# Kernel tuning notes

Measured on AMD Instinct MI355X. Metric: run time of the kernel, lower is better.

## Reference

```python
import jax, jax.numpy as jnp
import numpy as np

B, D, O = 131072, 128, 256

def setup_inputs() -> dict:
    key = jax.random.key(0)
    k1, k2, k3 = jax.random.split(key, 3)
    x = jax.random.normal(k1, (B, D), dtype=jnp.float32)
    weight = jax.random.normal(k2, (O, D), dtype=jnp.float32)
    bias = jax.random.normal(k3, (O,), dtype=jnp.float32)
    return {"x": x, "weight": weight, "bias": bias}

def reference(x, weight, bias):
    # Original: (x[:,None,:] * W[None,:,:]).sum(-1) == linear contraction over D.
    z = jnp.einsum('bd,od->bo', x, weight) + bias  # [B, O]
    # hyperoperation_order == 2 -> elementwise square; activation is None.
    return z * z
```

## Files before the change

kernel.cpp:

```cpp
#include <hip/hip_runtime.h>
#include <hip/hip_bf16.h>


#define B_ROWS 131072
#define D_DIM  128
#define O_DIM  256
#define ROWS_PER_BLOCK 128
#define THREADS 512
#define W_PITCH 136

using bf16x8 = __attribute__((ext_vector_type(8))) short;
using f32x4  = __attribute__((ext_vector_type(4))) float;

__device__ __forceinline__ short bf16bits(float f) {
    __hip_bfloat16 h = __float2bfloat16(f);
    return __builtin_bit_cast(short, h);
}

__global__ __launch_bounds__(THREADS, 4)
void hyper_linear_sq_kernel(const float* __restrict__ x,
                            const float* __restrict__ weight,
                            const float* __restrict__ bias,
                            float* __restrict__ out) {
    __shared__ short Wlds[O_DIM * W_PITCH];

    const int tid = threadIdx.x;

    {
        const float4* wv = (const float4*)weight;
        #pragma unroll
        for (int it = 0; it < 16; ++it) {
            int idx = it * THREADS + tid;
            float4 v = wv[idx];
            int e   = idx << 2;
            int row = e >> 7;
            int c   = e & 127;
            short4 p;
            p.x = bf16bits(v.x); p.y = bf16bits(v.y);
            p.z = bf16bits(v.z); p.w = bf16bits(v.w);
            *(short4*)&Wlds[row * W_PITCH + c] = p;
        }
    }

    const int lane = tid & 63;
    const int wid  = tid >> 6;
    const int n16  = lane & 15;
    const int quad = lane >> 4;

    const long rowbase = (long)blockIdx.x * ROWS_PER_BLOCK + wid * 16;

    const float* xr = x + (rowbase + n16) * D_DIM + quad * 8;
    bf16x8 a[4];
    #pragma unroll
    for (int ks = 0; ks < 4; ++ks) {
        float4 h0 = *(const float4*)(xr + ks * 32);
        float4 h1 = *(const float4*)(xr + ks * 32 + 4);
        bf16x8 t;
        t[0] = bf16bits(h0.x); t[1] = bf16bits(h0.y);
        t[2] = bf16bits(h0.z); t[3] = bf16bits(h0.w);
        t[4] = bf16bits(h1.x); t[5] = bf16bits(h1.y);
        t[6] = bf16bits(h1.z); t[7] = bf16bits(h1.w);
        a[ks] = t;
    }

    f32x4 acc[16];
    #pragma unroll
    for (int ct = 0; ct < 16; ++ct) acc[ct] = (f32x4){0.f, 0.f, 0.f, 0.f};

    __syncthreads();

    #pragma unroll
    for (int ks = 0; ks < 4; ++ks) {
        #pragma unroll
        for (int ct = 0; ct < 16; ++ct) {
            bf16x8 b = *(const bf16x8*)&Wlds[(ct * 16 + n16) * W_PITCH + ks * 32 + quad * 8];
            acc[ct] = __builtin_amdgcn_mfma_f32_16x16x32_bf16(a[ks], b, acc[ct], 0, 0, 0);
        }
    }

    #pragma unroll
    for (int ct = 0; ct < 16; ++ct) {
        int col = ct * 16 + n16;
        float bv = bias[col];
        #pragma unroll
        for (int r = 0; r < 4; ++r) {
            long row = rowbase + quad * 4 + r;
            float z = acc[ct][r] + bv;
            out[row * O_DIM + col] = z * z;
        }
    }
}

extern "C" void kernel_launch(void* const* d_in, const int* in_sizes, int n_in,
                              void* d_out, int out_size, void* d_ws, size_t ws_size,
                              hipStream_t stream) {
    const float* x    = (const float*)d_in[0];
    const float* w    = (const float*)d_in[1];
    const float* bias = (const float*)d_in[2];
    float* out        = (float*)d_out;
    dim3 grid(B_ROWS / ROWS_PER_BLOCK);
    hipLaunchKernelGGL(hyper_linear_sq_kernel, grid, dim3(THREADS), 0, stream,
                       x, w, bias, out);
}
```

Baseline: 189.1 us.

## Hold weight fragments in registers per wave, drop LDS, split columns across waves

Stops staging the full weight matrix in LDS. Each of four waves now owns 64 output columns and keeps its bf16 weight fragments and bias in registers, then loops over four 16-row tiles of x. This removes the LDS fill, the block barrier and the LDS reads. In exchange, every wave reloads the same x rows (four times per block) and reads weight from global or L2 once per block. It also replaces the library bf16 conversion with a manual round-to-nearest-even bit trick.

New measurement: 229.6 us. +21.4%, slower.

```diff
diff --git a/kernel.cpp b/kernel.cpp
--- a/kernel.cpp
+++ b/kernel.cpp
@@ -5,88 +5,91 @@
 #define B_ROWS 131072
 #define D_DIM  128
 #define O_DIM  256
-#define ROWS_PER_BLOCK 128
-#define THREADS 512
-#define W_PITCH 136
+#define THREADS 256
+#define NBLOCKS 2048
+#define ROWS_PER_BLOCK 64
+#define TILES (ROWS_PER_BLOCK / 16)
 
 using bf16x8 = __attribute__((ext_vector_type(8))) short;
 using f32x4  = __attribute__((ext_vector_type(4))) float;
 
-__device__ __forceinline__ short bf16bits(float f) {
-    __hip_bfloat16 h = __float2bfloat16(f);
-    return __builtin_bit_cast(short, h);
+__device__ __forceinline__ short bf16rne(float f) {
+    unsigned u = __builtin_bit_cast(unsigned, f);
+    u += 0x7FFFu + ((u >> 16) & 1u);
+    return (short)(u >> 16);
 }
 
-__global__ __launch_bounds__(THREADS, 4)
+__device__ __forceinline__ bf16x8 pack8(float4 h0, float4 h1) {
+    bf16x8 t;
+    t[0] = bf16rne(h0.x); t[1] = bf16rne(h0.y);
+    t[2] = bf16rne(h0.z); t[3] = bf16rne(h0.w);
+    t[4] = bf16rne(h1.x); t[5] = bf16rne(h1.y);
+    t[6] = bf16rne(h1.z); t[7] = bf16rne(h1.w);
+    return t;
+}
+
+__global__ __launch_bounds__(THREADS, 3)
 void hyper_linear_sq_kernel(const float* __restrict__ x,
                             const float* __restrict__ weight,
                             const float* __restrict__ bias,
                             float* __restrict__ out) {
-    __shared__ short Wlds[O_DIM * W_PITCH];
+    const int lane  = threadIdx.x & 63;
+    const int wid   = threadIdx.x >> 6;
+    const int n16   = lane & 15;
+    const int quad  = lane >> 4;
+    const int cbase = wid * 64;
 
-    const int tid = threadIdx.x;
-
-    {
-        const float4* wv = (const float4*)weight;
+    bf16x8 bfrag[4][4];
+    #pragma unroll
+    for (int ct = 0; ct < 4; ++ct) {
+        const float* wr = weight + (cbase + ct * 16 + n16) * D_DIM + quad * 8;
         #pragma unroll
-        for (int it = 0; it < 16; ++it) {
-            int idx = it * THREADS + tid;
-            float4 v = wv[idx];
-            int e   = idx << 2;
-            int row = e >> 7;
-            int c   = e & 127;
-            short4 p;
-            p.x = bf16bits(v.x); p.y = bf16bits(v.y);
-            p.z = bf16bits(v.z); p.w = bf16bits(v.w);
-            *(short4*)&Wlds[row * W_PITCH + c] = p;
+        for (int ks = 0; ks < 4; ++ks) {
+            float4 h0 = *(const float4*)(wr + ks * 32);
+            float4 h1 = *(const float4*)(wr + ks * 32 + 4);
+            bfrag[ct][ks] = pack8(h0, h1);
         }
     }
 
-    const int lane = tid & 63;
-    const int wid  = tid >> 6;
-    const int n16  = lane & 15;
-    const int quad = lane >> 4;
+    float bv[4];
+    #pragma unroll
+    for (int ct = 0; ct < 4; ++ct) bv[ct] = bias[cbase + ct * 16 + n16];
 
-    const long rowbase = (long)blockIdx.x * ROWS_PER_BLOCK + wid * 16;
+    const int rowbase0 = blockIdx.x * ROWS_PER_BLOCK;
 
-    const float* xr = x + (rowbase + n16) * D_DIM + quad * 8;
-    bf16x8 a[4];
-    #pragma unroll
-    for (int ks = 0; ks < 4; ++ks) {
-        float4 h0 = *(const float4*)(xr + ks * 32);
-        float4 h1 = *(const float4*)(xr + ks * 32 + 4);
-        bf16x8 t;
-        t[0] = bf16bits(h0.x); t[1] = bf16bits(h0.y);
-        t[2] = bf16bits(h0.z); t[3] = bf16bits(h0.w);
-        t[4] = bf16bits(h1.x); t[5] = bf16bits(h1.y);
-        t[6] = bf16bits(h1.z); t[7] = bf16bits(h1.w);
-        a[ks] = t;
-    }
+    for (int t = 0; t < TILES; ++t) {
+        const int rowbase = rowbase0 + t * 16;
 
-    f32x4 acc[16];
-    #pragma unroll
-    for (int ct = 0; ct < 16; ++ct) acc[ct] = (f32x4){0.f, 0.f, 0.f, 0.f};
+        const float* xr = x + (rowbase + n16) * D_DIM + quad * 8;
+        bf16x8 a[4];
+        #pragma unroll
+        for (int ks = 0; ks < 4; ++ks) {
+            float4 h0 = *(const float4*)(xr + ks * 32);
+            float4 h1 = *(const float4*)(xr + ks * 32 + 4);
+            a[ks] = pack8(h0, h1);
+        }
 
-    __syncthreads();
+        f32x4 acc[4];
+        #pragma unroll
+        for (int ct = 0; ct < 4; ++ct) acc[ct] = (f32x4){0.f, 0.f, 0.f, 0.f};
 
-    #pragma unroll
-    for (int ks = 0; ks < 4; ++ks) {
         #pragma unroll
-        for (int ct = 0; ct < 16; ++ct) {
-            bf16x8 b = *(const bf16x8*)&Wlds[(ct * 16 + n16) * W_PITCH + ks * 32 + quad * 8];
-            acc[ct] = __builtin_amdgcn_mfma_f32_16x16x32_bf16(a[ks], b, acc[ct], 0, 0, 0);
+        for (int ks = 0; ks < 4; ++ks) {
+            #pragma unroll
+            for (int ct = 0; ct < 4; ++ct) {
+                acc[ct] = __builtin_amdgcn_mfma_f32_16x16x32_bf16(a[ks], bfrag[ct][ks], acc[ct], 0, 0, 0);
+            }
         }
-    }
 
-    #pragma unroll
-    for (int ct = 0; ct < 16; ++ct) {
-        int col = ct * 16 + n16;
-        float bv = bias[col];
         #pragma unroll
-        for (int r = 0; r < 4; ++r) {
-            long row = rowbase + quad * 4 + r;
-            float z = acc[ct][r] + bv;
-            out[row * O_DIM + col] = z * z;
+        for (int ct = 0; ct < 4; ++ct) {
+            const int col = cbase + ct * 16 + n16;
+            #pragma unroll
+            for (int r = 0; r < 4; ++r) {
+                const int row = rowbase + quad * 4 + r;
+                float z = acc[ct][r] + bv[ct];
+                out[row * O_DIM + col] = z * z;
+            }
         }
     }
 }
@@ -98,7 +101,6 @@
     const float* w    = (const float*)d_in[1];
     const float* bias = (const float*)d_in[2];
     float* out        = (float*)d_out;
-    dim3 grid(B_ROWS / ROWS_PER_BLOCK);
-    hipLaunchKernelGGL(hyper_linear_sq_kernel, grid, dim3(THREADS), 0, stream,
+    hipLaunchKernelGGL(hyper_linear_sq_kernel, dim3(NBLOCKS), dim3(THREADS), 0, stream,
                        x, w, bias, out);
 }
```
